# Performance work log

Hardware: AMD Instinct MI355X
Metric: run time of the kernel (lower is better)

Reference implementation:

```python
import jax, jax.numpy as jnp
import numpy as np

NUM_HEADS = 16
HEAD_DIM = 64  # hidden_dim 1024 / 16 heads
COH_DIM = 8
MOT_RANK = 4


def _linear(x, W, b):
    # torch nn.Linear: y = x @ W.T + b
    return jnp.einsum('...i,oi->...o', x, W) + b


def setup_inputs() -> dict:
    key = jax.random.key(0)
    ks = jax.random.split(key, 17)
    d, c, m = HEAD_DIM, COH_DIM, MOT_RANK
    s = 1.0 / np.sqrt(d)
    sc = 1.0 / np.sqrt(c)
    sm = 1.0 / np.sqrt(m)
    inp = {
        'x': jax.random.normal(ks[0], (4, 2048, 1024), dtype=jnp.float32),
        'Wi': jax.random.uniform(ks[1], (d, d), jnp.float32, -s, s),
        'bi': jax.random.uniform(ks[2], (d,), jnp.float32, -s, s),
        'Wq': jax.random.uniform(ks[3], (d, d), jnp.float32, -s, s),
        'bq': jax.random.uniform(ks[4], (d,), jnp.float32, -s, s),
        'Wk': jax.random.uniform(ks[5], (d, d), jnp.float32, -s, s),
        'bk': jax.random.uniform(ks[6], (d,), jnp.float32, -s, s),
        'Wv': jax.random.uniform(ks[7], (d, d), jnp.float32, -s, s),
        'bv': jax.random.uniform(ks[8], (d,), jnp.float32, -s, s),
        'Wc': jax.random.uniform(ks[9], (c, d), jnp.float32, -s, s),
        'bc': jax.random.uniform(ks[10], (c,), jnp.float32, -s, s),
        'Wci': jax.random.uniform(ks[11], (d, c), jnp.float32, -sc, sc),
        'bci': jax.random.uniform(ks[12], (d,), jnp.float32, -sc, sc),
        'Wm': jax.random.uniform(ks[13], (m, d), jnp.float32, -s, s),
        'bm': jax.random.uniform(ks[14], (m,), jnp.float32, -s, s),
        'Wmi': jax.random.uniform(ks[15], (d, m), jnp.float32, -sm, sm),
        'bmi': jax.random.uniform(ks[16], (d,), jnp.float32, -sm, sm),
    }
    return inp


def reference(x, Wi, bi, Wq, bq, Wk, bk, Wv, bv, Wc, bc, Wci, bci, Wm, bm, Wmi, bmi):
    B, S, D = x.shape
    H, hd = NUM_HEADS, HEAD_DIM
    # split heads: [B, H, S, hd]
    xh = x.reshape(B, S, H, hd).transpose(0, 2, 1, 3)
    # resolution * load_factor = 1.0 scaling (identity here), then input projection
    h = _linear(xh, Wi, bi)
    q = _linear(h, Wq, bq)
    k = _linear(h, Wk, bk)
    v = _linear(h, Wv, bv)
    # scaled dot-product attention per head
    scores = jnp.einsum('bhqd,bhkd->bhqk', q, k) / jnp.sqrt(jnp.float32(hd))
    attn = jax.nn.softmax(scores, axis=-1)
    out = jnp.einsum('bhqk,bhkd->bhqd', attn, v)
    # cohomology round-trip projection
    out = _linear(_linear(out, Wc, bc), Wci, bci)
    # motive round-trip projection
    out = _linear(_linear(out, Wm, bm), Wmi, bmi)
    # merge heads back to [B, S, D]
    return out.transpose(0, 2, 1, 3).reshape(B, S, D)
```

## Files before the change

### kernel.cpp

```cpp
#include <hip/hip_runtime.h>


#define SEQ 2048
#define DM  1024
#define HD  64
#define QS  0.180336880111120429f

typedef short bf16x8 __attribute__((ext_vector_type(8)));
typedef unsigned short u16x8 __attribute__((ext_vector_type(8)));
typedef float f32x16 __attribute__((ext_vector_type(16)));

#define MFMA32 __builtin_amdgcn_mfma_f32_32x32x16_bf16

#if defined(__has_builtin)
#if __has_builtin(__builtin_amdgcn_exp2f)
#define EXP2(x) __builtin_amdgcn_exp2f(x)
#endif
#endif
#ifndef EXP2
#define EXP2(x) exp2f(x)
#endif

#define KG_OFF  12288
#define VG_OFF  (12288 + 8388608)
#define WS_NEED ((size_t)512 + 2ull * (12288 + 2ull * 8388608))

__device__ __forceinline__ unsigned short f2bf(float f) {
    unsigned int v = __float_as_uint(f);
    unsigned int r = v + 0x7FFFu + ((v >> 16) & 1u);
    return (unsigned short)(r >> 16);
}
__device__ __forceinline__ unsigned int pk2r(float a, float b) {
    return __builtin_amdgcn_perm(__float_as_uint(b) + 0x8000u,
                                 __float_as_uint(a) + 0x8000u, 0x07060302u);
}
__device__ __forceinline__ unsigned int pk2t(float a, float b) {
    return __builtin_amdgcn_perm(__float_as_uint(b), __float_as_uint(a), 0x07060302u);
}
__device__ __forceinline__ f32x16 z16() {
    f32x16 v;
    #pragma unroll
    for (int i = 0; i < 16; i++) v[i] = 0.f;
    return v;
}

__device__ __forceinline__ void mm16L(const float* __restrict__ wrow,
                                      const float* __restrict__ L, int i0,
                                      float* __restrict__ acc) {
    #pragma unroll
    for (int ii = 0; ii < 16; ii++) acc[ii] = 0.f;
    for (int t = 0; t < 64; t += 4) {
        float4 w4 = *(const float4*)(wrow + t);
        #pragma unroll
        for (int d = 0; d < 4; d++) {
            float wv = (d == 0) ? w4.x : (d == 1) ? w4.y : (d == 2) ? w4.z : w4.w;
            const float* lr = L + (t + d) * 68 + i0;
            float4 a = *(const float4*)lr;
            float4 b = *(const float4*)(lr + 4);
            float4 c = *(const float4*)(lr + 8);
            float4 e = *(const float4*)(lr + 12);
            acc[0] += wv * a.x;  acc[1] += wv * a.y;  acc[2]  += wv * a.z;  acc[3]  += wv * a.w;
            acc[4] += wv * b.x;  acc[5] += wv * b.y;  acc[6]  += wv * b.z;  acc[7]  += wv * b.w;
            acc[8] += wv * c.x;  acc[9] += wv * c.y;  acc[10] += wv * c.z;  acc[11] += wv * c.w;
            acc[12] += wv * e.x; acc[13] += wv * e.y; acc[14] += wv * e.z;  acc[15] += wv * e.w;
        }
    }
}

__global__ __launch_bounds__(256)
void qmt_combine(const float* __restrict__ Wi,  const float* __restrict__ bi,
                 const float* __restrict__ Wq,  const float* __restrict__ bq,
                 const float* __restrict__ Wk,  const float* __restrict__ bk,
                 const float* __restrict__ Wv,  const float* __restrict__ bv,
                 const float* __restrict__ Wc,  const float* __restrict__ bc,
                 const float* __restrict__ Wci, const float* __restrict__ bci,
                 const float* __restrict__ Wm,  const float* __restrict__ bm,
                 const float* __restrict__ Wmi, const float* __restrict__ bmi,
                 float* __restrict__ ws) {
    const int tid = threadIdx.x;
    const int o = tid & 63;
    const int i0 = (tid >> 6) * 16;
    const bool lead = (tid < 64);

    __shared__ float Wi_s[64 * 68];
    __shared__ float Wq_s[64 * 68];
    __shared__ float Wk_s[64 * 68];
    __shared__ float Wv_s[64 * 68];
    __shared__ float Wvi_s[64 * 68];
    __shared__ float M_s[64 * 68];
    __shared__ float Wc_s[512];
    __shared__ float Wci_s[512];
    __shared__ float Wm_s[256];
    __shared__ float Wmi_s[256];
    __shared__ float bi_s[64], bvi_s[64], c1[64], c2[4];
    __shared__ float U1[32], U2[256];

    unsigned short* wsu = (unsigned short*)(ws + 128);

    for (int i4 = tid; i4 < 1024; i4 += 256) {
        int r = i4 >> 4, c = (i4 & 15) * 4;
        *(float4*)&Wi_s[r * 68 + c] = *(const float4*)(Wi + i4 * 4);
        *(float4*)&Wq_s[r * 68 + c] = *(const float4*)(Wq + i4 * 4);
        *(float4*)&Wk_s[r * 68 + c] = *(const float4*)(Wk + i4 * 4);
        *(float4*)&Wv_s[r * 68 + c] = *(const float4*)(Wv + i4 * 4);
    }
    if (tid < 128) {
        *(float4*)&Wc_s[tid * 4]  = *(const float4*)(Wc + tid * 4);
        *(float4*)&Wci_s[tid * 4] = *(const float4*)(Wci + tid * 4);
    } else if (tid < 192) {
        int t = tid - 128;
        *(float4*)&Wm_s[t * 4]  = *(const float4*)(Wm + t * 4);
        *(float4*)&Wmi_s[t * 4] = *(const float4*)(Wmi + t * 4);
    }
    if (lead) bi_s[o] = bi[o];
    __syncthreads();

    float acc[16];
    mm16L(Wq_s + o * 68, Wi_s, i0, acc);
    #pragma unroll
    for (int ii = 0; ii < 16; ii++) wsu[o * 64 + i0 + ii] = f2bf(acc[ii] * QS);
    if (lead) {
        float s = bq[o];
        for (int t = 0; t < 64; t++) s += Wq_s[o * 68 + t] * bi_s[t];
        ws[o] = s * QS;
    }
    mm16L(Wk_s + o * 68, Wi_s, i0, acc);
    #pragma unroll
    for (int ii = 0; ii < 16; ii++) wsu[4096 + o * 64 + i0 + ii] = f2bf(acc[ii]);
    mm16L(Wv_s + o * 68, Wi_s, i0, acc);
    #pragma unroll
    for (int ii = 0; ii < 16; ii++) Wvi_s[o * 68 + i0 + ii] = acc[ii];
    if (lead) {
        float s = bv[o];
        for (int t = 0; t < 64; t++) s += Wv_s[o * 68 + t] * bi_s[t];
        bvi_s[o] = s;
    }
    if (tid < 32) {
        int a = tid >> 3, c = tid & 7;
        float s = 0.f;
        for (int t = 0; t < 64; t++) s += Wm_s[a * 64 + t] * Wci_s[t * 8 + c];
        U1[a * 8 + c] = s;
    }
    __syncthreads();
    if (lead) {
        for (int a = 0; a < 4; a++) {
            float s = 0.f;
            for (int cc = 0; cc < 8; cc++) s += U1[a * 8 + cc] * Wc_s[cc * 64 + o];
            U2[a * 64 + o] = s;
        }
        float s = bci[o];
        for (int j = 0; j < 8; j++) s += Wci_s[o * 8 + j] * bc[j];
        c1[o] = s;
    }
    __syncthreads();
    #pragma unroll
    for (int ii = 0; ii < 16; ii++) {
        float s = 0.f;
        for (int a = 0; a < 4; a++) s += Wmi_s[o * 4 + a] * U2[a * 64 + i0 + ii];
        M_s[o * 68 + i0 + ii] = s;
    }
    if (tid < 4) {
        float s = bm[tid];
        for (int i = 0; i < 64; i++) s += Wm_s[tid * 64 + i] * c1[i];
        c2[tid] = s;
    }
    __syncthreads();
    mm16L(M_s + o * 68, Wvi_s, i0, acc);
    #pragma unroll
    for (int ii = 0; ii < 16; ii++) wsu[8192 + o * 64 + i0 + ii] = f2bf(acc[ii]);
    if (lead) {
        float bvv = 0.f;
        for (int t = 0; t < 64; t++) bvv += M_s[o * 68 + t] * bvi_s[t];
        float cvv = bmi[o];
        for (int a = 0; a < 4; a++) cvv += Wmi_s[o * 4 + a] * c2[a];
        ws[64 + o] = cvv + bvv;
    }
}

__global__ __launch_bounds__(256)
void qmt_kv(const float* __restrict__ x, float* __restrict__ ws) {
    const int tid = threadIdx.x;
    const int w = tid >> 6;
    const int lane = tid & 63;
    const int ln = lane & 31;
    const int h = lane >> 5;
    const int b = blockIdx.y >> 4;
    const int hh = blockIdx.y & 15;

    const unsigned short* wsu = (const unsigned short*)(ws + 128);
    unsigned short* Kg = (unsigned short*)(ws + 128) + KG_OFF + (size_t)blockIdx.y * (2048 * 64);
    unsigned short* Vg = (unsigned short*)(ws + 128) + VG_OFF + (size_t)blockIdx.y * (64 * 2048);

    const int krl = (w >> 1) * 32 + ln;
    const int dt32 = (w & 1) * 32;

    bf16x8 akf[4], avf[4];
    #pragma unroll
    for (int c = 0; c < 4; c++) {
        int row = dt32 + ln;
        int col = c * 16 + h * 8;
        akf[c] = *(const bf16x8*)(wsu + 4096 + row * 64 + col);
        avf[c] = *(const bf16x8*)(wsu + 8192 + row * 64 + col);
    }
    for (int t = 0; t < 4; t++) {
        const int kt = blockIdx.x * 4 + t;
        bf16x8 xf[4];
        const float* xr = x + ((size_t)(b * SEQ + kt * 64 + krl) * DM + hh * HD);
        #pragma unroll
        for (int c = 0; c < 4; c++) {
            const float* p = xr + c * 16 + h * 8;
            float4 f0 = *(const float4*)p;
            float4 f1 = *(const float4*)(p + 4);
            union { bf16x8 v; unsigned int u[4]; } tt;
            tt.u[0] = pk2t(f0.x, f0.y); tt.u[1] = pk2t(f0.z, f0.w);
            tt.u[2] = pk2t(f1.x, f1.y); tt.u[3] = pk2t(f1.z, f1.w);
            xf[c] = tt.v;
        }
        f32x16 kacc = z16(), vacc = z16();
        #pragma unroll
        for (int c = 0; c < 4; c++) kacc = MFMA32(akf[c], xf[c], kacc, 0, 0, 0);
        #pragma unroll
        for (int c = 0; c < 4; c++) vacc = MFMA32(xf[c], avf[c], vacc, 0, 0, 0);
        #pragma unroll
        for (int g = 0; g < 4; g++) {
            uint2 pk_, pv_;
            pk_.x = pk2r(kacc[4 * g + 0], kacc[4 * g + 1]);
            pk_.y = pk2r(kacc[4 * g + 2], kacc[4 * g + 3]);
            *(uint2*)&Kg[(size_t)(kt * 64 + krl) * 64 + dt32 + 8 * g + 4 * h] = pk_;
            pv_.x = pk2r(vacc[4 * g + 0], vacc[4 * g + 1]);
            pv_.y = pk2r(vacc[4 * g + 2], vacc[4 * g + 3]);
            *(uint2*)&Vg[(size_t)(dt32 + ln) * 2048 + kt * 64 + (w >> 1) * 32 + 8 * g + 4 * h] = pv_;
        }
    }
}

__global__ __launch_bounds__(256, 4)
void qmt_attn2(const float* __restrict__ x, const float* __restrict__ wsf,
               float* __restrict__ out) {
    __shared__ __align__(16) unsigned short ps_s[128 * 72];
    __shared__ __align__(16) unsigned short ks_s[64 * 72];
    __shared__ __align__(16) unsigned short vt_s[64 * 72];
    __shared__ float als_l[128];
    __shared__ float ls_l[128];

    const int tid = threadIdx.x;
    const int w = tid >> 6;
    const int lane = tid & 63;
    const int ln = lane & 31;
    const int h = lane >> 5;
    const int b = blockIdx.y >> 4;
    const int hh = blockIdx.y & 15;
    const int qbase = blockIdx.x * 128;

    const unsigned short* wsu = (const unsigned short*)(wsf + 128);
    const unsigned short* Kg = wsu + KG_OFF + (size_t)blockIdx.y * (2048 * 64);
    const unsigned short* Vg = wsu + VG_OFF + (size_t)blockIdx.y * (64 * 2048);

    const float ec0 = wsf[64 + ln];
    const float ec1 = wsf[96 + ln];

    bf16x8 qf[4];
    {
        bf16x8 xq[4];
        const float* xrow = x + ((size_t)(b * SEQ + qbase + w * 32 + ln) * DM + hh * HD);
        #pragma unroll
        for (int c = 0; c < 4; c++) {
            const float* p = xrow + c * 16 + h * 8;
            float4 f0 = *(const float4*)p;
            float4 f1 = *(const float4*)(p + 4);
            union { bf16x8 v; unsigned int u[4]; } t;
            t.u[0] = pk2t(f0.x, f0.y); t.u[1] = pk2t(f0.z, f0.w);
            t.u[2] = pk2t(f1.x, f1.y); t.u[3] = pk2t(f1.z, f1.w);
            xq[c] = t.v;
        }
        #pragma unroll
        for (int m = 0; m < 2; m++) {
            f32x16 acc;
            #pragma unroll
            for (int g = 0; g < 4; g++) {
                float4 b4 = *(const float4*)&wsf[m * 32 + 8 * g + 4 * h];
                acc[4 * g + 0] = b4.x; acc[4 * g + 1] = b4.y;
                acc[4 * g + 2] = b4.z; acc[4 * g + 3] = b4.w;
            }
            #pragma unroll
            for (int c = 0; c < 4; c++) {
                bf16x8 aq = *(const bf16x8*)(wsu + (m * 32 + ln) * 64 + c * 16 + h * 8);
                acc = MFMA32(aq, xq[c], acc, 0, 0, 0);
            }
            #pragma unroll
            for (int g = 0; g < 4; g++) {
                uint2 pw;
                pw.x = pk2r(acc[4 * g + 0], acc[4 * g + 1]);
                pw.y = pk2r(acc[4 * g + 2], acc[4 * g + 3]);
                *(uint2*)&ps_s[(w * 32 + ln) * 72 + m * 32 + 8 * g + 4 * h] = pw;
            }
        }
        #pragma unroll
        for (int c = 0; c < 4; c++)
            qf[c] = *(const bf16x8*)&ps_s[(w * 32 + ln) * 72 + c * 16 + h * 8];
    }

    f32x16 o0 = z16(), o1 = z16();
    float m_i = -1e30f, l_i = 0.f;

    const int srow = tid >> 3;
    const int scol = (tid & 7) * 8;

    u16x8 ka, kb, va, vb;
    ka = *(const u16x8*)(Kg + (size_t)srow * 64 + scol);
    kb = *(const u16x8*)(Kg + (size_t)(srow + 32) * 64 + scol);
    va = *(const u16x8*)(Vg + (size_t)srow * 2048 + scol);
    vb = *(const u16x8*)(Vg + (size_t)(srow + 32) * 2048 + scol);
    *(u16x8*)&ks_s[srow * 72 + scol] = ka;
    *(u16x8*)&ks_s[(srow + 32) * 72 + scol] = kb;
    *(u16x8*)&vt_s[srow * 72 + scol] = va;
    *(u16x8*)&vt_s[(srow + 32) * 72 + scol] = vb;
    __syncthreads();

    for (int kt = 0; kt < SEQ / 64; kt++) {
        const bool more = (kt < SEQ / 64 - 1);
        if (more) {
            const int kn = (kt + 1) * 64;
            ka = *(const u16x8*)(Kg + (size_t)(kn + srow) * 64 + scol);
            kb = *(const u16x8*)(Kg + (size_t)(kn + srow + 32) * 64 + scol);
            va = *(const u16x8*)(Vg + (size_t)srow * 2048 + kn + scol);
            vb = *(const u16x8*)(Vg + (size_t)(srow + 32) * 2048 + kn + scol);
        }

        f32x16 st0 = z16(), st1 = z16();
        #pragma unroll
        for (int c = 0; c < 4; c++) {
            bf16x8 k0 = *(const bf16x8*)&ks_s[ln * 72 + c * 16 + h * 8];
            bf16x8 k1 = *(const bf16x8*)&ks_s[(32 + ln) * 72 + c * 16 + h * 8];
            st0 = MFMA32(k0, qf[c], st0, 0, 0, 0);
            st1 = MFMA32(k1, qf[c], st1, 0, 0, 0);
        }
        float mx = st0[0];
        #pragma unroll
        for (int i = 1; i < 16; i++) mx = fmaxf(mx, st0[i]);
        #pragma unroll
        for (int i = 0; i < 16; i++) mx = fmaxf(mx, st1[i]);
        mx = fmaxf(mx, __shfl_xor(mx, 32));
        const float mn = fmaxf(m_i, mx);
        const float al = EXP2(m_i - mn);
        float ss = 0.f;
        #pragma unroll
        for (int i = 0; i < 16; i++) { st0[i] = EXP2(st0[i] - mn); ss += st0[i]; }
        #pragma unroll
        for (int i = 0; i < 16; i++) { st1[i] = EXP2(st1[i] - mn); ss += st1[i]; }
        ss += __shfl_xor(ss, 32);
        l_i = l_i * al + ss;
        m_i = mn;
        if (lane < 32) als_l[w * 32 + lane] = al;
        #pragma unroll
        for (int g = 0; g < 4; g++) {
            uint2 p0, p1;
            p0.x = pk2r(st0[4 * g + 0], st0[4 * g + 1]);
            p0.y = pk2r(st0[4 * g + 2], st0[4 * g + 3]);
            *(uint2*)&ps_s[(w * 32 + ln) * 72 + 8 * g + 4 * h] = p0;
            p1.x = pk2r(st1[4 * g + 0], st1[4 * g + 1]);
            p1.y = pk2r(st1[4 * g + 2], st1[4 * g + 3]);
            *(uint2*)&ps_s[(w * 32 + ln) * 72 + 32 + 8 * g + 4 * h] = p1;
        }
        #pragma unroll
        for (int g = 0; g < 4; g++) {
            float4 a4 = *(const float4*)&als_l[w * 32 + 8 * g + 4 * h];
            o0[4 * g + 0] *= a4.x; o0[4 * g + 1] *= a4.y;
            o0[4 * g + 2] *= a4.z; o0[4 * g + 3] *= a4.w;
            o1[4 * g + 0] *= a4.x; o1[4 * g + 1] *= a4.y;
            o1[4 * g + 2] *= a4.z; o1[4 * g + 3] *= a4.w;
        }
        #pragma unroll
        for (int c = 0; c < 4; c++) {
            bf16x8 pf = *(const bf16x8*)&ps_s[(w * 32 + ln) * 72 + c * 16 + h * 8];
            bf16x8 v0 = *(const bf16x8*)&vt_s[ln * 72 + c * 16 + h * 8];
            bf16x8 v1 = *(const bf16x8*)&vt_s[(32 + ln) * 72 + c * 16 + h * 8];
            o0 = MFMA32(pf, v0, o0, 0, 0, 0);
            o1 = MFMA32(pf, v1, o1, 0, 0, 0);
        }
        __syncthreads();
        if (more) {
            *(u16x8*)&ks_s[srow * 72 + scol] = ka;
            *(u16x8*)&ks_s[(srow + 32) * 72 + scol] = kb;
            *(u16x8*)&vt_s[srow * 72 + scol] = va;
            *(u16x8*)&vt_s[(srow + 32) * 72 + scol] = vb;
        }
        __syncthreads();
    }

    if (lane < 32) ls_l[w * 32 + lane] = l_i;
    #pragma unroll
    for (int g = 0; g < 4; g++) {
        float4 l4 = *(const float4*)&ls_l[w * 32 + 8 * g + 4 * h];
        float4 iv = make_float4(1.f / l4.x, 1.f / l4.y, 1.f / l4.z, 1.f / l4.w);
        #pragma unroll
        for (int i = 0; i < 4; i++) {
            float ivv = (i == 0) ? iv.x : (i == 1) ? iv.y : (i == 2) ? iv.z : iv.w;
            int q = qbase + w * 32 + 8 * g + 4 * h + i;
            float* orow = out + ((size_t)(b * SEQ + q) * DM + hh * HD);
            orow[ln] = o0[4 * g + i] * ivv + ec0;
            orow[32 + ln] = o1[4 * g + i] * ivv + ec1;
        }
    }
}

__global__ __launch_bounds__(256, 3)
void qmt_attn_fb(const float* __restrict__ x, const float* __restrict__ wsf,
                 float* __restrict__ out) {
    __shared__ __align__(16) unsigned short ps_s[128 * 72];
    __shared__ __align__(16) unsigned short ks_s[64 * 72];
    __shared__ __align__(16) unsigned short vt_s[64 * 72];
    __shared__ float als_l[128];
    __shared__ float ls_l[128];

    const int tid = threadIdx.x;
    const int w = tid >> 6;
    const int lane = tid & 63;
    const int ln = lane & 31;
    const int h = lane >> 5;
    const int b = blockIdx.y >> 4;
    const int hh = blockIdx.y & 15;
    const int qbase = blockIdx.x * 128;

    const unsigned short* wsu = (const unsigned short*)(wsf + 128);

    bf16x8 akf[4], avf[4];
    #pragma unroll
    for (int c = 0; c < 4; c++) {
        int row = (w & 1) * 32 + ln;
        int col = c * 16 + h * 8;
        akf[c] = *(const bf16x8*)(wsu + 4096 + row * 64 + col);
        avf[c] = *(const bf16x8*)(wsu + 8192 + row * 64 + col);
    }
    const float ec0 = wsf[64 + ln];
    const float ec1 = wsf[96 + ln];

    bf16x8 qf[4];
    {
        bf16x8 xq[4];
        const float* xrow = x + ((size_t)(b * SEQ + qbase + w * 32 + ln) * DM + hh * HD);
        #pragma unroll
        for (int c = 0; c < 4; c++) {
            const float* p = xrow + c * 16 + h * 8;
            float4 f0 = *(const float4*)p;
            float4 f1 = *(const float4*)(p + 4);
            union { bf16x8 v; unsigned int u[4]; } t;
            t.u[0] = pk2t(f0.x, f0.y); t.u[1] = pk2t(f0.z, f0.w);
            t.u[2] = pk2t(f1.x, f1.y); t.u[3] = pk2t(f1.z, f1.w);
            xq[c] = t.v;
        }
        #pragma unroll
        for (int m = 0; m < 2; m++) {
            f32x16 acc;
            #pragma unroll
            for (int g = 0; g < 4; g++) {
                float4 b4 = *(const float4*)&wsf[m * 32 + 8 * g + 4 * h];
                acc[4 * g + 0] = b4.x; acc[4 * g + 1] = b4.y;
                acc[4 * g + 2] = b4.z; acc[4 * g + 3] = b4.w;
            }
            #pragma unroll
            for (int c = 0; c < 4; c++) {
                bf16x8 aq = *(const bf16x8*)(wsu + (m * 32 + ln) * 64 + c * 16 + h * 8);
                acc = MFMA32(aq, xq[c], acc, 0, 0, 0);
            }
            #pragma unroll
            for (int g = 0; g < 4; g++) {
                uint2 pw;
                pw.x = pk2r(acc[4 * g + 0], acc[4 * g + 1]);
                pw.y = pk2r(acc[4 * g + 2], acc[4 * g + 3]);
                *(uint2*)&ps_s[(w * 32 + ln) * 72 + m * 32 + 8 * g + 4 * h] = pw;
            }
        }
        #pragma unroll
        for (int c = 0; c < 4; c++)
            qf[c] = *(const bf16x8*)&ps_s[(w * 32 + ln) * 72 + c * 16 + h * 8];
    }

    f32x16 o0 = z16(), o1 = z16();
    float m_i = -1e30f, l_i = 0.f;

    const int krl = (w >> 1) * 32 + ln;
    const int dt32 = (w & 1) * 32;

    for (int kt = 0; kt < SEQ / 64; kt++) {
        bf16x8 xf[4];
        const float* xr = x + ((size_t)(b * SEQ + kt * 64 + krl) * DM + hh * HD);
        #pragma unroll
        for (int c = 0; c < 4; c++) {
            const float* p = xr + c * 16 + h * 8;
            float4 f0 = *(const float4*)p;
            float4 f1 = *(const float4*)(p + 4);
            union { bf16x8 v; unsigned int u[4]; } t;
            t.u[0] = pk2t(f0.x, f0.y); t.u[1] = pk2t(f0.z, f0.w);
            t.u[2] = pk2t(f1.x, f1.y); t.u[3] = pk2t(f1.z, f1.w);
            xf[c] = t.v;
        }
        f32x16 kacc = z16(), vacc = z16();
        #pragma unroll
        for (int c = 0; c < 4; c++) kacc = MFMA32(akf[c], xf[c], kacc, 0, 0, 0);
        #pragma unroll
        for (int c = 0; c < 4; c++) vacc = MFMA32(xf[c], avf[c], vacc, 0, 0, 0);
        #pragma unroll
        for (int g = 0; g < 4; g++) {
            uint2 pk_, pv_;
            pk_.x = pk2r(kacc[4 * g + 0], kacc[4 * g + 1]);
            pk_.y = pk2r(kacc[4 * g + 2], kacc[4 * g + 3]);
            *(uint2*)&ks_s[krl * 72 + dt32 + 8 * g + 4 * h] = pk_;
            pv_.x = pk2r(vacc[4 * g + 0], vacc[4 * g + 1]);
            pv_.y = pk2r(vacc[4 * g + 2], vacc[4 * g + 3]);
            *(uint2*)&vt_s[(dt32 + ln) * 72 + (w >> 1) * 32 + 8 * g + 4 * h] = pv_;
        }
        __syncthreads();

        f32x16 st0 = z16(), st1 = z16();
        #pragma unroll
        for (int c = 0; c < 4; c++) {
            bf16x8 k0 = *(const bf16x8*)&ks_s[ln * 72 + c * 16 + h * 8];
            bf16x8 k1 = *(const bf16x8*)&ks_s[(32 + ln) * 72 + c * 16 + h * 8];
            st0 = MFMA32(k0, qf[c], st0, 0, 0, 0);
            st1 = MFMA32(k1, qf[c], st1, 0, 0, 0);
        }
        float mx = st0[0];
        #pragma unroll
        for (int i = 1; i < 16; i++) mx = fmaxf(mx, st0[i]);
        #pragma unroll
        for (int i = 0; i < 16; i++) mx = fmaxf(mx, st1[i]);
        mx = fmaxf(mx, __shfl_xor(mx, 32));
        const float mn = fmaxf(m_i, mx);
        const float al = EXP2(m_i - mn);
        float ss = 0.f;
        #pragma unroll
        for (int i = 0; i < 16; i++) { st0[i] = EXP2(st0[i] - mn); ss += st0[i]; }
        #pragma unroll
        for (int i = 0; i < 16; i++) { st1[i] = EXP2(st1[i] - mn); ss += st1[i]; }
        ss += __shfl_xor(ss, 32);
        l_i = l_i * al + ss;
        m_i = mn;
        if (lane < 32) als_l[w * 32 + lane] = al;
        #pragma unroll
        for (int g = 0; g < 4; g++) {
            uint2 p0, p1;
            p0.x = pk2r(st0[4 * g + 0], st0[4 * g + 1]);
            p0.y = pk2r(st0[4 * g + 2], st0[4 * g + 3]);
            *(uint2*)&ps_s[(w * 32 + ln) * 72 + 8 * g + 4 * h] = p0;
            p1.x = pk2r(st1[4 * g + 0], st1[4 * g + 1]);
            p1.y = pk2r(st1[4 * g + 2], st1[4 * g + 3]);
            *(uint2*)&ps_s[(w * 32 + ln) * 72 + 32 + 8 * g + 4 * h] = p1;
        }
        #pragma unroll
        for (int g = 0; g < 4; g++) {
            float4 a4 = *(const float4*)&als_l[w * 32 + 8 * g + 4 * h];
            o0[4 * g + 0] *= a4.x; o0[4 * g + 1] *= a4.y;
            o0[4 * g + 2] *= a4.z; o0[4 * g + 3] *= a4.w;
            o1[4 * g + 0] *= a4.x; o1[4 * g + 1] *= a4.y;
            o1[4 * g + 2] *= a4.z; o1[4 * g + 3] *= a4.w;
        }
        #pragma unroll
        for (int c = 0; c < 4; c++) {
            bf16x8 pf = *(const bf16x8*)&ps_s[(w * 32 + ln) * 72 + c * 16 + h * 8];
            bf16x8 v0 = *(const bf16x8*)&vt_s[ln * 72 + c * 16 + h * 8];
            bf16x8 v1 = *(const bf16x8*)&vt_s[(32 + ln) * 72 + c * 16 + h * 8];
            o0 = MFMA32(pf, v0, o0, 0, 0, 0);
            o1 = MFMA32(pf, v1, o1, 0, 0, 0);
        }
        __syncthreads();
    }

    if (lane < 32) ls_l[w * 32 + lane] = l_i;
    #pragma unroll
    for (int g = 0; g < 4; g++) {
        float4 l4 = *(const float4*)&ls_l[w * 32 + 8 * g + 4 * h];
        float4 iv = make_float4(1.f / l4.x, 1.f / l4.y, 1.f / l4.z, 1.f / l4.w);
        #pragma unroll
        for (int i = 0; i < 4; i++) {
            float ivv = (i == 0) ? iv.x : (i == 1) ? iv.y : (i == 2) ? iv.z : iv.w;
            int q = qbase + w * 32 + 8 * g + 4 * h + i;
            float* orow = out + ((size_t)(b * SEQ + q) * DM + hh * HD);
            orow[ln] = o0[4 * g + i] * ivv + ec0;
            orow[32 + ln] = o1[4 * g + i] * ivv + ec1;
        }
    }
}

extern "C" void kernel_launch(void* const* d_in, const int* in_sizes, int n_in,
                              void* d_out, int out_size, void* d_ws, size_t ws_size,
                              hipStream_t stream) {
    const float* x = (const float*)d_in[0];
    float* wsf = (float*)d_ws;

    qmt_combine<<<1, 256, 0, stream>>>(
        (const float*)d_in[1],  (const float*)d_in[2],
        (const float*)d_in[3],  (const float*)d_in[4],
        (const float*)d_in[5],  (const float*)d_in[6],
        (const float*)d_in[7],  (const float*)d_in[8],
        (const float*)d_in[9],  (const float*)d_in[10],
        (const float*)d_in[11], (const float*)d_in[12],
        (const float*)d_in[13], (const float*)d_in[14],
        (const float*)d_in[15], (const float*)d_in[16],
        wsf);

    if (ws_size >= WS_NEED) {
        dim3 gkv(SEQ / 256, 64);
        qmt_kv<<<gkv, 256, 0, stream>>>(x, wsf);
        dim3 grid(SEQ / 128, 64);
        qmt_attn2<<<grid, 256, 0, stream>>>(x, wsf, (float*)d_out);
    } else {
        dim3 grid(SEQ / 128, 64);
        qmt_attn_fb<<<grid, 256, 0, stream>>>(x, wsf, (float*)d_out);
    }
}
```

Before: 247.2 us.

## Rework attention kernel: register P/Q fragments, lazy rescale, swizzled LDS, split combine

The main attention kernel now keeps Q and P fragments in registers, using hardware bf16 pack plus permlane32 swaps, instead of round-tripping them through shared memory. It skips the output rescale unless the running max grows past a threshold, and swaps padded K/V tiles for XOR-swizzled ones. It also splits the weight-combine kernel across three blocks and launches the K/V projection with one tile per block. These changes target LDS traffic, per-tile exp/rescale work and serial prologue latency, at the cost of inline asm that depends on the gfx950 instruction set and a thresholded softmax max that changes rounding behaviour.

After: 243.1 us. About the same (-1.7%).

```diff
diff --git a/kernel.cpp b/kernel.cpp
--- a/kernel.cpp
+++ b/kernel.cpp
@@ -5,6 +5,7 @@
 #define DM  1024
 #define HD  64
 #define QS  0.180336880111120429f
+#define THR 8.0f
 
 typedef short bf16x8 __attribute__((ext_vector_type(8)));
 typedef unsigned short u16x8 __attribute__((ext_vector_type(8)));
@@ -37,11 +38,30 @@
 __device__ __forceinline__ unsigned int pk2t(float a, float b) {
     return __builtin_amdgcn_perm(__float_as_uint(b), __float_as_uint(a), 0x07060302u);
 }
+__device__ __forceinline__ unsigned int cvtpk(float a, float b) {
+    unsigned int r;
+    asm("v_cvt_pk_bf16_f32 %0, %1, %2" : "=v"(r) : "v"(a), "v"(b));
+    return r;
+}
+__device__ __forceinline__ void swap32(unsigned int& a, unsigned int& b) {
+    asm("v_permlane32_swap_b32 %0, %1" : "+v"(a), "+v"(b));
+}
 __device__ __forceinline__ f32x16 z16() {
     f32x16 v;
     #pragma unroll
     for (int i = 0; i < 16; i++) v[i] = 0.f;
     return v;
+}
+
+__device__ __forceinline__ void pack2(const f32x16 s, bf16x8& fA, bf16x8& fB) {
+    union { bf16x8 v; unsigned int u[4]; } a, b;
+    a.u[0] = cvtpk(s[0], s[1]);   a.u[1] = cvtpk(s[2], s[3]);
+    a.u[2] = cvtpk(s[4], s[5]);   a.u[3] = cvtpk(s[6], s[7]);
+    b.u[0] = cvtpk(s[8], s[9]);   b.u[1] = cvtpk(s[10], s[11]);
+    b.u[2] = cvtpk(s[12], s[13]); b.u[3] = cvtpk(s[14], s[15]);
+    swap32(a.u[0], a.u[2]); swap32(a.u[1], a.u[3]);
+    swap32(b.u[0], b.u[2]); swap32(b.u[1], b.u[3]);
+    fA = a.v; fB = b.v;
 }
 
 __device__ __forceinline__ void mm16L(const float* __restrict__ wrow,
@@ -81,11 +101,10 @@
     const int o = tid & 63;
     const int i0 = (tid >> 6) * 16;
     const bool lead = (tid < 64);
-
+    const int role = blockIdx.x;
+
+    __shared__ float Wa_s[64 * 68];
     __shared__ float Wi_s[64 * 68];
-    __shared__ float Wq_s[64 * 68];
-    __shared__ float Wk_s[64 * 68];
-    __shared__ float Wv_s[64 * 68];
     __shared__ float Wvi_s[64 * 68];
     __shared__ float M_s[64 * 68];
     __shared__ float Wc_s[512];
@@ -96,43 +115,50 @@
     __shared__ float U1[32], U2[256];
 
     unsigned short* wsu = (unsigned short*)(ws + 128);
+    const float* Wa = (role == 0) ? Wq : (role == 1) ? Wk : Wv;
 
     for (int i4 = tid; i4 < 1024; i4 += 256) {
         int r = i4 >> 4, c = (i4 & 15) * 4;
         *(float4*)&Wi_s[r * 68 + c] = *(const float4*)(Wi + i4 * 4);
-        *(float4*)&Wq_s[r * 68 + c] = *(const float4*)(Wq + i4 * 4);
-        *(float4*)&Wk_s[r * 68 + c] = *(const float4*)(Wk + i4 * 4);
-        *(float4*)&Wv_s[r * 68 + c] = *(const float4*)(Wv + i4 * 4);
-    }
-    if (tid < 128) {
-        *(float4*)&Wc_s[tid * 4]  = *(const float4*)(Wc + tid * 4);
-        *(float4*)&Wci_s[tid * 4] = *(const float4*)(Wci + tid * 4);
-    } else if (tid < 192) {
-        int t = tid - 128;
-        *(float4*)&Wm_s[t * 4]  = *(const float4*)(Wm + t * 4);
-        *(float4*)&Wmi_s[t * 4] = *(const float4*)(Wmi + t * 4);
+        *(float4*)&Wa_s[r * 68 + c] = *(const float4*)(Wa + i4 * 4);
+    }
+    if (role == 2) {
+        if (tid < 128) {
+            *(float4*)&Wc_s[tid * 4]  = *(const float4*)(Wc + tid * 4);
+            *(float4*)&Wci_s[tid * 4] = *(const float4*)(Wci + tid * 4);
+        } else if (tid < 192) {
+            int t = tid - 128;
+            *(float4*)&Wm_s[t * 4]  = *(const float4*)(Wm + t * 4);
+            *(float4*)&Wmi_s[t * 4] = *(const float4*)(Wmi + t * 4);
+        }
     }
     if (lead) bi_s[o] = bi[o];
     __syncthreads();
 
     float acc[16];
-    mm16L(Wq_s + o * 68, Wi_s, i0, acc);
-    #pragma unroll
-    for (int ii = 0; ii < 16; ii++) wsu[o * 64 + i0 + ii] = f2bf(acc[ii] * QS);
-    if (lead) {
-        float s = bq[o];
-        for (int t = 0; t < 64; t++) s += Wq_s[o * 68 + t] * bi_s[t];
-        ws[o] = s * QS;
-    }
-    mm16L(Wk_s + o * 68, Wi_s, i0, acc);
-    #pragma unroll
-    for (int ii = 0; ii < 16; ii++) wsu[4096 + o * 64 + i0 + ii] = f2bf(acc[ii]);
-    mm16L(Wv_s + o * 68, Wi_s, i0, acc);
+    if (role == 0) {
+        mm16L(Wa_s + o * 68, Wi_s, i0, acc);
+        #pragma unroll
+        for (int ii = 0; ii < 16; ii++) wsu[o * 64 + i0 + ii] = f2bf(acc[ii] * QS);
+        if (lead) {
+            float s = bq[o];
+            for (int t = 0; t < 64; t++) s += Wa_s[o * 68 + t] * bi_s[t];
+            ws[o] = s * QS;
+        }
+        return;
+    }
+    if (role == 1) {
+        mm16L(Wa_s + o * 68, Wi_s, i0, acc);
+        #pragma unroll
+        for (int ii = 0; ii < 16; ii++) wsu[4096 + o * 64 + i0 + ii] = f2bf(acc[ii]);
+        return;
+    }
+    mm16L(Wa_s + o * 68, Wi_s, i0, acc);
     #pragma unroll
     for (int ii = 0; ii < 16; ii++) Wvi_s[o * 68 + i0 + ii] = acc[ii];
     if (lead) {
         float s = bv[o];
-        for (int t = 0; t < 64; t++) s += Wv_s[o * 68 + t] * bi_s[t];
+        for (int t = 0; t < 64; t++) s += Wa_s[o * 68 + t] * bi_s[t];
         bvi_s[o] = s;
     }
     if (tid < 32) {
@@ -186,6 +212,7 @@
     const int h = lane >> 5;
     const int b = blockIdx.y >> 4;
     const int hh = blockIdx.y & 15;
+    const int kt = blockIdx.x;
 
     const unsigned short* wsu = (const unsigned short*)(ws + 128);
     unsigned short* Kg = (unsigned short*)(ws + 128) + KG_OFF + (size_t)blockIdx.y * (2048 * 64);
@@ -202,44 +229,40 @@
         akf[c] = *(const bf16x8*)(wsu + 4096 + row * 64 + col);
         avf[c] = *(const bf16x8*)(wsu + 8192 + row * 64 + col);
     }
-    for (int t = 0; t < 4; t++) {
-        const int kt = blockIdx.x * 4 + t;
-        bf16x8 xf[4];
-        const float* xr = x + ((size_t)(b * SEQ + kt * 64 + krl) * DM + hh * HD);
-        #pragma unroll
-        for (int c = 0; c < 4; c++) {
-            const float* p = xr + c * 16 + h * 8;
-            float4 f0 = *(const float4*)p;
-            float4 f1 = *(const float4*)(p + 4);
-            union { bf16x8 v; unsigned int u[4]; } tt;
-            tt.u[0] = pk2t(f0.x, f0.y); tt.u[1] = pk2t(f0.z, f0.w);
-            tt.u[2] = pk2t(f1.x, f1.y); tt.u[3] = pk2t(f1.z, f1.w);
-            xf[c] = tt.v;
-        }
-        f32x16 kacc = z16(), vacc = z16();
-        #pragma unroll
-        for (int c = 0; c < 4; c++) kacc = MFMA32(akf[c], xf[c], kacc, 0, 0, 0);
-        #pragma unroll
-        for (int c = 0; c < 4; c++) vacc = MFMA32(xf[c], avf[c], vacc, 0, 0, 0);
-        #pragma unroll
-        for (int g = 0; g < 4; g++) {
-            uint2 pk_, pv_;
-            pk_.x = pk2r(kacc[4 * g + 0], kacc[4 * g + 1]);
-            pk_.y = pk2r(kacc[4 * g + 2], kacc[4 * g + 3]);
-            *(uint2*)&Kg[(size_t)(kt * 64 + krl) * 64 + dt32 + 8 * g + 4 * h] = pk_;
-            pv_.x = pk2r(vacc[4 * g + 0], vacc[4 * g + 1]);
-            pv_.y = pk2r(vacc[4 * g + 2], vacc[4 * g + 3]);
-            *(uint2*)&Vg[(size_t)(dt32 + ln) * 2048 + kt * 64 + (w >> 1) * 32 + 8 * g + 4 * h] = pv_;
-        }
+    bf16x8 xf[4];
+    const float* xr = x + ((size_t)(b * SEQ + kt * 64 + krl) * DM + hh * HD);
+    #pragma unroll
+    for (int c = 0; c < 4; c++) {
+        const float* p = xr + c * 16 + h * 8;
+        float4 f0 = *(const float4*)p;
+        float4 f1 = *(const float4*)(p + 4);
+        union { bf16x8 v; unsigned int u[4]; } tt;
+        tt.u[0] = pk2t(f0.x, f0.y); tt.u[1] = pk2t(f0.z, f0.w);
+        tt.u[2] = pk2t(f1.x, f1.y); tt.u[3] = pk2t(f1.z, f1.w);
+        xf[c] = tt.v;
+    }
+    f32x16 kacc = z16(), vacc = z16();
+    #pragma unroll
+    for (int c = 0; c < 4; c++) kacc = MFMA32(akf[c], xf[c], kacc, 0, 0, 0);
+    #pragma unroll
+    for (int c = 0; c < 4; c++) vacc = MFMA32(xf[c], avf[c], vacc, 0, 0, 0);
+    #pragma unroll
+    for (int g = 0; g < 4; g++) {
+        uint2 pk_, pv_;
+        pk_.x = cvtpk(kacc[4 * g + 0], kacc[4 * g + 1]);
+        pk_.y = cvtpk(kacc[4 * g + 2], kacc[4 * g + 3]);
+        *(uint2*)&Kg[(size_t)(kt * 64 + krl) * 64 + dt32 + 8 * g + 4 * h] = pk_;
+        pv_.x = cvtpk(vacc[4 * g + 0], vacc[4 * g + 1]);
+        pv_.y = cvtpk(vacc[4 * g + 2], vacc[4 * g + 3]);
+        *(uint2*)&Vg[(size_t)(dt32 + ln) * 2048 + kt * 64 + (w >> 1) * 32 + 8 * g + 4 * h] = pv_;
     }
 }
 
 __global__ __launch_bounds__(256, 4)
 void qmt_attn2(const float* __restrict__ x, const float* __restrict__ wsf,
                float* __restrict__ out) {
-    __shared__ __align__(16) unsigned short ps_s[128 * 72];
-    __shared__ __align__(16) unsigned short ks_s[64 * 72];
-    __shared__ __align__(16) unsigned short vt_s[64 * 72];
+    __shared__ __align__(16) unsigned short ks_s[64 * 64];
+    __shared__ __align__(16) unsigned short vt_s[64 * 64];
     __shared__ float als_l[128];
     __shared__ float ls_l[128];
 
@@ -256,6 +279,189 @@
     const unsigned short* Kg = wsu + KG_OFF + (size_t)blockIdx.y * (2048 * 64);
     const unsigned short* Vg = wsu + VG_OFF + (size_t)blockIdx.y * (64 * 2048);
 
+    const float ec0 = wsf[64 + ln];
+    const float ec1 = wsf[96 + ln];
+
+    const int srow = tid >> 3;
+    const int scol = (tid & 7) * 8;
+    const int sch = (((tid & 7) ^ (srow & 7)) * 8);
+    const int swm = ln & 7;
+
+    u16x8 ka = *(const u16x8*)(Kg + (size_t)srow * 64 + scol);
+    u16x8 kb = *(const u16x8*)(Kg + (size_t)(srow + 32) * 64 + scol);
+    u16x8 va = *(const u16x8*)(Vg + (size_t)srow * 2048 + scol);
+    u16x8 vb = *(const u16x8*)(Vg + (size_t)(srow + 32) * 2048 + scol);
+
+    bf16x8 qf[4];
+    {
+        bf16x8 xq[4];
+        const float* xrow = x + ((size_t)(b * SEQ + qbase + w * 32 + ln) * DM + hh * HD);
+        #pragma unroll
+        for (int c = 0; c < 4; c++) {
+            const float* p = xrow + c * 16 + h * 8;
+            float4 f0 = *(const float4*)p;
+            float4 f1 = *(const float4*)(p + 4);
+            union { bf16x8 v; unsigned int u[4]; } t;
+            t.u[0] = pk2t(f0.x, f0.y); t.u[1] = pk2t(f0.z, f0.w);
+            t.u[2] = pk2t(f1.x, f1.y); t.u[3] = pk2t(f1.z, f1.w);
+            xq[c] = t.v;
+        }
+        #pragma unroll
+        for (int m = 0; m < 2; m++) {
+            f32x16 acc;
+            #pragma unroll
+            for (int g = 0; g < 4; g++) {
+                float4 b4 = *(const float4*)&wsf[m * 32 + 8 * g + 4 * h];
+                acc[4 * g + 0] = b4.x; acc[4 * g + 1] = b4.y;
+                acc[4 * g + 2] = b4.z; acc[4 * g + 3] = b4.w;
+            }
+            #pragma unroll
+            for (int c = 0; c < 4; c++) {
+                bf16x8 aq = *(const bf16x8*)(wsu + (m * 32 + ln) * 64 + c * 16 + h * 8);
+                acc = MFMA32(aq, xq[c], acc, 0, 0, 0);
+            }
+            pack2(acc, qf[2 * m], qf[2 * m + 1]);
+        }
+    }
+
+    f32x16 o0 = z16(), o1 = z16();
+    float m_i = -1e30f, l_i = 0.f;
+
+    *(u16x8*)&ks_s[srow * 64 + sch] = ka;
+    *(u16x8*)&ks_s[(srow + 32) * 64 + sch] = kb;
+    *(u16x8*)&vt_s[srow * 64 + sch] = va;
+    *(u16x8*)&vt_s[(srow + 32) * 64 + sch] = vb;
+    __syncthreads();
+
+    for (int kt = 0; kt < SEQ / 64; kt++) {
+        const bool more = (kt < SEQ / 64 - 1);
+        if (more) {
+            const int kn = (kt + 1) * 64;
+            ka = *(const u16x8*)(Kg + (size_t)(kn + srow) * 64 + scol);
+            kb = *(const u16x8*)(Kg + (size_t)(kn + srow + 32) * 64 + scol);
+            va = *(const u16x8*)(Vg + (size_t)srow * 2048 + kn + scol);
+            vb = *(const u16x8*)(Vg + (size_t)(srow + 32) * 2048 + kn + scol);
+        }
+
+        f32x16 st0 = z16(), st1 = z16();
+        #pragma unroll
+        for (int c = 0; c < 4; c++) {
+            const int ci = ((c * 2 + h) ^ swm) * 8;
+            bf16x8 k0 = *(const bf16x8*)&ks_s[ln * 64 + ci];
+            bf16x8 k1 = *(const bf16x8*)&ks_s[(32 + ln) * 64 + ci];
+            st0 = MFMA32(k0, qf[c], st0, 0, 0, 0);
+            st1 = MFMA32(k1, qf[c], st1, 0, 0, 0);
+        }
+
+        float tm[8];
+        #pragma unroll
+        for (int i = 0; i < 8; i++)
+            tm[i] = fmaxf(fmaxf(st0[i], st0[i + 8]), fmaxf(st1[i], st1[i + 8]));
+        #pragma unroll
+        for (int i = 0; i < 4; i++) tm[i] = fmaxf(tm[i], tm[i + 4]);
+        float mx = fmaxf(fmaxf(tm[0], tm[1]), fmaxf(tm[2], tm[3]));
+        mx = fmaxf(mx, __shfl_xor(mx, 32));
+
+        const bool need = __any(mx > m_i + THR) != 0;
+        float mn = m_i, al = 1.0f;
+        if (need) {
+            mn = fmaxf(m_i, mx);
+            al = EXP2(m_i - mn);
+            if (lane < 32) als_l[w * 32 + lane] = al;
+        }
+
+        #pragma unroll
+        for (int i = 0; i < 16; i++) st0[i] = EXP2(st0[i] - mn);
+        #pragma unroll
+        for (int i = 0; i < 16; i++) st1[i] = EXP2(st1[i] - mn);
+        float sm[8];
+        #pragma unroll
+        for (int i = 0; i < 8; i++)
+            sm[i] = (st0[i] + st0[i + 8]) + (st1[i] + st1[i + 8]);
+        #pragma unroll
+        for (int i = 0; i < 4; i++) sm[i] += sm[i + 4];
+        float ss = (sm[0] + sm[1]) + (sm[2] + sm[3]);
+        ss += __shfl_xor(ss, 32);
+        l_i = l_i * al + ss;
+        m_i = mn;
+
+        bf16x8 pf[4];
+        pack2(st0, pf[0], pf[1]);
+        pack2(st1, pf[2], pf[3]);
+
+        if (need) {
+            #pragma unroll
+            for (int g = 0; g < 4; g++) {
+                float4 a4 = *(const float4*)&als_l[w * 32 + 8 * g + 4 * h];
+                o0[4 * g + 0] *= a4.x; o0[4 * g + 1] *= a4.y;
+                o0[4 * g + 2] *= a4.z; o0[4 * g + 3] *= a4.w;
+                o1[4 * g + 0] *= a4.x; o1[4 * g + 1] *= a4.y;
+                o1[4 * g + 2] *= a4.z; o1[4 * g + 3] *= a4.w;
+            }
+        }
+
+        #pragma unroll
+        for (int c = 0; c < 4; c++) {
+            const int ci = ((c * 2 + h) ^ swm) * 8;
+            bf16x8 v0 = *(const bf16x8*)&vt_s[ln * 64 + ci];
+            bf16x8 v1 = *(const bf16x8*)&vt_s[(32 + ln) * 64 + ci];
+            o0 = MFMA32(pf[c], v0, o0, 0, 0, 0);
+            o1 = MFMA32(pf[c], v1, o1, 0, 0, 0);
+        }
+        __syncthreads();
+        if (more) {
+            *(u16x8*)&ks_s[srow * 64 + sch] = ka;
+            *(u16x8*)&ks_s[(srow + 32) * 64 + sch] = kb;
+            *(u16x8*)&vt_s[srow * 64 + sch] = va;
+            *(u16x8*)&vt_s[(srow + 32) * 64 + sch] = vb;
+        }
+        __syncthreads();
+    }
+
+    if (lane < 32) ls_l[w * 32 + lane] = l_i;
+    #pragma unroll
+    for (int g = 0; g < 4; g++) {
+        float4 l4 = *(const float4*)&ls_l[w * 32 + 8 * g + 4 * h];
+        float4 iv = make_float4(1.f / l4.x, 1.f / l4.y, 1.f / l4.z, 1.f / l4.w);
+        #pragma unroll
+        for (int i = 0; i < 4; i++) {
+            float ivv = (i == 0) ? iv.x : (i == 1) ? iv.y : (i == 2) ? iv.z : iv.w;
+            int q = qbase + w * 32 + 8 * g + 4 * h + i;
+            float* orow = out + ((size_t)(b * SEQ + q) * DM + hh * HD);
+            orow[ln] = o0[4 * g + i] * ivv + ec0;
+            orow[32 + ln] = o1[4 * g + i] * ivv + ec1;
+        }
+    }
+}
+
+__global__ __launch_bounds__(256, 3)
+void qmt_attn_fb(const float* __restrict__ x, const float* __restrict__ wsf,
+                 float* __restrict__ out) {
+    __shared__ __align__(16) unsigned short ps_s[128 * 72];
+    __shared__ __align__(16) unsigned short ks_s[64 * 72];
+    __shared__ __align__(16) unsigned short vt_s[64 * 72];
+    __shared__ float als_l[128];
+    __shared__ float ls_l[128];
+
+    const int tid = threadIdx.x;
+    const int w = tid >> 6;
+    const int lane = tid & 63;
+    const int ln = lane & 31;
+    const int h = lane >> 5;
+    const int b = blockIdx.y >> 4;
+    const int hh = blockIdx.y & 15;
+    const int qbase = blockIdx.x * 128;
+
+    const unsigned short* wsu = (const unsigned short*)(wsf + 128);
+
+    bf16x8 akf[4], avf[4];
+    #pragma unroll
+    for (int c = 0; c < 4; c++) {
+        int row = (w & 1) * 32 + ln;
+        int col = c * 16 + h * 8;
+        akf[c] = *(const bf16x8*)(wsu + 4096 + row * 64 + col);
+        avf[c] = *(const bf16x8*)(wsu + 8192 + row * 64 + col);
+    }
     const float ec0 = wsf[64 + ln];
     const float ec1 = wsf[96 + ln];
 
@@ -303,29 +509,38 @@
     f32x16 o0 = z16(), o1 = z16();
     float m_i = -1e30f, l_i = 0.f;
 
-    const int srow = tid >> 3;
-    const int scol = (tid & 7) * 8;
-
-    u16x8 ka, kb, va, vb;
-    ka = *(const u16x8*)(Kg + (size_t)srow * 64 + scol);
-    kb = *(const u16x8*)(Kg + (size_t)(srow + 32) * 64 + scol);
-    va = *(const u16x8*)(Vg + (size_t)srow * 2048 + scol);
-    vb = *(const u16x8*)(Vg + (size_t)(srow + 32) * 2048 + scol);
-    *(u16x8*)&ks_s[srow * 72 + scol] = ka;
-    *(u16x8*)&ks_s[(srow + 32) * 72 + scol] = kb;
-    *(u16x8*)&vt_s[srow * 72 + scol] = va;
-    *(u16x8*)&vt_s[(srow + 32) * 72 + scol] = vb;
-    __syncthreads();
+    const int krl = (w >> 1) * 32 + ln;
+    const int dt32 = (w & 1) * 32;
 
     for (int kt = 0; kt < SEQ / 64; kt++) {
-        const bool more = (kt < SEQ / 64 - 1);
-        if (more) {
-            const int kn = (kt + 1) * 64;
-            ka = *(const u16x8*)(Kg + (size_t)(kn + srow) * 64 + scol);
-            kb = *(const u16x8*)(Kg + (size_t)(kn + srow + 32) * 64 + scol);
-            va = *(const u16x8*)(Vg + (size_t)srow * 2048 + kn + scol);
-            vb = *(const u16x8*)(Vg + (size_t)(srow + 32) * 2048 + kn + scol);
-        }
+        bf16x8 xf[4];
+        const float* xr = x + ((size_t)(b * SEQ + kt * 64 + krl) * DM + hh * HD);
+        #pragma unroll
+        for (int c = 0; c < 4; c++) {
+            const float* p = xr + c * 16 + h * 8;
+            float4 f0 = *(const float4*)p;
+            float4 f1 = *(const float4*)(p + 4);
+            union { bf16x8 v; unsigned int u[4]; } t;
+            t.u[0] = pk2t(f0.x, f0.y); t.u[1] = pk2t(f0.z, f0.w);
+            t.u[2] = pk2t(f1.x, f1.y); t.u[3] = pk2t(f1.z, f1.w);
+            xf[c] = t.v;
+        }
+        f32x16 kacc = z16(), vacc = z16();
+        #pragma unroll
+        for (int c = 0; c < 4; c++) kacc = MFMA32(akf[c], xf[c], kacc, 0, 0, 0);
+        #pragma unroll
+        for (int c = 0; c < 4; c++) vacc = MFMA32(xf[c], avf[c], vacc, 0, 0, 0);
+        #pragma unroll
+        for (int g = 0; g < 4; g++) {
+            uint2 pk_, pv_;
+            pk_.x = pk2r(kacc[4 * g + 0], kacc[4 * g + 1]);
+            pk_.y = pk2r(kacc[4 * g + 2], kacc[4 * g + 3]);
+            *(uint2*)&ks_s[krl * 72 + dt32 + 8 * g + 4 * h] = pk_;
+            pv_.x = pk2r(vacc[4 * g + 0], vacc[4 * g + 1]);
+            pv_.y = pk2r(vacc[4 * g + 2], vacc[4 * g + 3]);
+            *(uint2*)&vt_s[(dt32 + ln) * 72 + (w >> 1) * 32 + 8 * g + 4 * h] = pv_;
+        }
+        __syncthreads();
 
         f32x16 st0 = z16(), st1 = z16();
         #pragma unroll
@@ -379,13 +594,6 @@
             o1 = MFMA32(pf, v1, o1, 0, 0, 0);
         }
         __syncthreads();
-        if (more) {
-            *(u16x8*)&ks_s[srow * 72 + scol] = ka;
-            *(u16x8*)&ks_s[(srow + 32) * 72 + scol] = kb;
-            *(u16x8*)&vt_s[srow * 72 + scol] = va;
-            *(u16x8*)&vt_s[(srow + 32) * 72 + scol] = vb;
-        }
-        __syncthreads();
     }
 
     if (lane < 32) ls_l[w * 32 + lane] = l_i;
@@ -404,191 +612,13 @@
     }
 }
 
-__global__ __launch_bounds__(256, 3)
-void qmt_attn_fb(const float* __restrict__ x, const float* __restrict__ wsf,
-                 float* __restrict__ out) {
-    __shared__ __align__(16) unsigned short ps_s[128 * 72];
-    __shared__ __align__(16) unsigned short ks_s[64 * 72];
-    __shared__ __align__(16) unsigned short vt_s[64 * 72];
-    __shared__ float als_l[128];
-    __shared__ float ls_l[128];
-
-    const int tid = threadIdx.x;
-    const int w = tid >> 6;
-    const int lane = tid & 63;
-    const int ln = lane & 31;
-    const int h = lane >> 5;
-    const int b = blockIdx.y >> 4;
-    const int hh = blockIdx.y & 15;
-    const int qbase = blockIdx.x * 128;
-
-    const unsigned short* wsu = (const unsigned short*)(wsf + 128);
-
-    bf16x8 akf[4], avf[4];
-    #pragma unroll
-    for (int c = 0; c < 4; c++) {
-        int row = (w & 1) * 32 + ln;
-        int col = c * 16 + h * 8;
-        akf[c] = *(const bf16x8*)(wsu + 4096 + row * 64 + col);
-        avf[c] = *(const bf16x8*)(wsu + 8192 + row * 64 + col);
-    }
-    const float ec0 = wsf[64 + ln];
-    const float ec1 = wsf[96 + ln];
-
-    bf16x8 qf[4];
-    {
-        bf16x8 xq[4];
-        const float* xrow = x + ((size_t)(b * SEQ + qbase + w * 32 + ln) * DM + hh * HD);
-        #pragma unroll
-        for (int c = 0; c < 4; c++) {
-            const float* p = xrow + c * 16 + h * 8;
-            float4 f0 = *(const float4*)p;
-            float4 f1 = *(const float4*)(p + 4);
-            union { bf16x8 v; unsigned int u[4]; } t;
-            t.u[0] = pk2t(f0.x, f0.y); t.u[1] = pk2t(f0.z, f0.w);
-            t.u[2] = pk2t(f1.x, f1.y); t.u[3] = pk2t(f1.z, f1.w);
-            xq[c] = t.v;
-        }
-        #pragma unroll
-        for (int m = 0; m < 2; m++) {
-            f32x16 acc;
-            #pragma unroll
-            for (int g = 0; g < 4; g++) {
-                float4 b4 = *(const float4*)&wsf[m * 32 + 8 * g + 4 * h];
-                acc[4 * g + 0] = b4.x; acc[4 * g + 1] = b4.y;
-                acc[4 * g + 2] = b4.z; acc[4 * g + 3] = b4.w;
-            }
-            #pragma unroll
-            for (int c = 0; c < 4; c++) {
-                bf16x8 aq = *(const bf16x8*)(wsu + (m * 32 + ln) * 64 + c * 16 + h * 8);
-                acc = MFMA32(aq, xq[c], acc, 0, 0, 0);
-            }
-            #pragma unroll
-            for (int g = 0; g < 4; g++) {
-                uint2 pw;
-                pw.x = pk2r(acc[4 * g + 0], acc[4 * g + 1]);
-                pw.y = pk2r(acc[4 * g + 2], acc[4 * g + 3]);
-                *(uint2*)&ps_s[(w * 32 + ln) * 72 + m * 32 + 8 * g + 4 * h] = pw;
-            }
-        }
-        #pragma unroll
-        for (int c = 0; c < 4; c++)
-            qf[c] = *(const bf16x8*)&ps_s[(w * 32 + ln) * 72 + c * 16 + h * 8];
-    }
-
-    f32x16 o0 = z16(), o1 = z16();
-    float m_i = -1e30f, l_i = 0.f;
-
-    const int krl = (w >> 1) * 32 + ln;
-    const int dt32 = (w & 1) * 32;
-
-    for (int kt = 0; kt < SEQ / 64; kt++) {
-        bf16x8 xf[4];
-        const float* xr = x + ((size_t)(b * SEQ + kt * 64 + krl) * DM + hh * HD);
-        #pragma unroll
-        for (int c = 0; c < 4; c++) {
-            const float* p = xr + c * 16 + h * 8;
-            float4 f0 = *(const float4*)p;
-            float4 f1 = *(const float4*)(p + 4);
-            union { bf16x8 v; unsigned int u[4]; } t;
-            t.u[0] = pk2t(f0.x, f0.y); t.u[1] = pk2t(f0.z, f0.w);
-            t.u[2] = pk2t(f1.x, f1.y); t.u[3] = pk2t(f1.z, f1.w);
-            xf[c] = t.v;
-        }
-        f32x16 kacc = z16(), vacc = z16();
-        #pragma unroll
-        for (int c = 0; c < 4; c++) kacc = MFMA32(akf[c], xf[c], kacc, 0, 0, 0);
-        #pragma unroll
-        for (int c = 0; c < 4; c++) vacc = MFMA32(xf[c], avf[c], vacc, 0, 0, 0);
-        #pragma unroll
-        for (int g = 0; g < 4; g++) {
-            uint2 pk_, pv_;
-            pk_.x = pk2r(kacc[4 * g + 0], kacc[4 * g + 1]);
-            pk_.y = pk2r(kacc[4 * g + 2], kacc[4 * g + 3]);
-            *(uint2*)&ks_s[krl * 72 + dt32 + 8 * g + 4 * h] = pk_;
-            pv_.x = pk2r(vacc[4 * g + 0], vacc[4 * g + 1]);
-            pv_.y = pk2r(vacc[4 * g + 2], vacc[4 * g + 3]);
-            *(uint2*)&vt_s[(dt32 + ln) * 72 + (w >> 1) * 32 + 8 * g + 4 * h] = pv_;
-        }
-        __syncthreads();
-
-        f32x16 st0 = z16(), st1 = z16();
-        #pragma unroll
-        for (int c = 0; c < 4; c++) {
-            bf16x8 k0 = *(const bf16x8*)&ks_s[ln * 72 + c * 16 + h * 8];
-            bf16x8 k1 = *(const bf16x8*)&ks_s[(32 + ln) * 72 + c * 16 + h * 8];
-            st0 = MFMA32(k0, qf[c], st0, 0, 0, 0);
-            st1 = MFMA32(k1, qf[c], st1, 0, 0, 0);
-        }
-        float mx = st0[0];
-        #pragma unroll
-        for (int i = 1; i < 16; i++) mx = fmaxf(mx, st0[i]);
-        #pragma unroll
-        for (int i = 0; i < 16; i++) mx = fmaxf(mx, st1[i]);
-        mx = fmaxf(mx, __shfl_xor(mx, 32));
-        const float mn = fmaxf(m_i, mx);
-        const float al = EXP2(m_i - mn);
-        float ss = 0.f;
-        #pragma unroll
-        for (int i = 0; i < 16; i++) { st0[i] = EXP2(st0[i] - mn); ss += st0[i]; }
-        #pragma unroll
-        for (int i = 0; i < 16; i++) { st1[i] = EXP2(st1[i] - mn); ss += st1[i]; }
-        ss += __shfl_xor(ss, 32);
-        l_i = l_i * al + ss;
-        m_i = mn;
-        if (lane < 32) als_l[w * 32 + lane] = al;
-        #pragma unroll
-        for (int g = 0; g < 4; g++) {
-            uint2 p0, p1;
-            p0.x = pk2r(st0[4 * g + 0], st0[4 * g + 1]);
-            p0.y = pk2r(st0[4 * g + 2], st0[4 * g + 3]);
-            *(uint2*)&ps_s[(w * 32 + ln) * 72 + 8 * g + 4 * h] = p0;
-            p1.x = pk2r(st1[4 * g + 0], st1[4 * g + 1]);
-            p1.y = pk2r(st1[4 * g + 2], st1[4 * g + 3]);
-            *(uint2*)&ps_s[(w * 32 + ln) * 72 + 32 + 8 * g + 4 * h] = p1;
-        }
-        #pragma unroll
-        for (int g = 0; g < 4; g++) {
-            float4 a4 = *(const float4*)&als_l[w * 32 + 8 * g + 4 * h];
-            o0[4 * g + 0] *= a4.x; o0[4 * g + 1] *= a4.y;
-            o0[4 * g + 2] *= a4.z; o0[4 * g + 3] *= a4.w;
-            o1[4 * g + 0] *= a4.x; o1[4 * g + 1] *= a4.y;
-            o1[4 * g + 2] *= a4.z; o1[4 * g + 3] *= a4.w;
-        }
-        #pragma unroll
-        for (int c = 0; c < 4; c++) {
-            bf16x8 pf = *(const bf16x8*)&ps_s[(w * 32 + ln) * 72 + c * 16 + h * 8];
-            bf16x8 v0 = *(const bf16x8*)&vt_s[ln * 72 + c * 16 + h * 8];
-            bf16x8 v1 = *(const bf16x8*)&vt_s[(32 + ln) * 72 + c * 16 + h * 8];
-            o0 = MFMA32(pf, v0, o0, 0, 0, 0);
-            o1 = MFMA32(pf, v1, o1, 0, 0, 0);
-        }
-        __syncthreads();
-    }
-
-    if (lane < 32) ls_l[w * 32 + lane] = l_i;
-    #pragma unroll
-    for (int g = 0; g < 4; g++) {
-        float4 l4 = *(const float4*)&ls_l[w * 32 + 8 * g + 4 * h];
-        float4 iv = make_float4(1.f / l4.x, 1.f / l4.y, 1.f / l4.z, 1.f / l4.w);
-        #pragma unroll
-        for (int i = 0; i < 4; i++) {
-            float ivv = (i == 0) ? iv.x : (i == 1) ? iv.y : (i == 2) ? iv.z : iv.w;
-            int q = qbase + w * 32 + 8 * g + 4 * h + i;
-            float* orow = out + ((size_t)(b * SEQ + q) * DM + hh * HD);
-            orow[ln] = o0[4 * g + i] * ivv + ec0;
-            orow[32 + ln] = o1[4 * g + i] * ivv + ec1;
-        }
-    }
-}
-
 extern "C" void kernel_launch(void* const* d_in, const int* in_sizes, int n_in,
                               void* d_out, int out_size, void* d_ws, size_t ws_size,
                               hipStream_t stream) {
     const float* x = (const float*)d_in[0];
     float* wsf = (float*)d_ws;
 
-    qmt_combine<<<1, 256, 0, stream>>>(
+    qmt_combine<<<3, 256, 0, stream>>>(
         (const float*)d_in[1],  (const float*)d_in[2],
         (const float*)d_in[3],  (const float*)d_in[4],
         (const float*)d_in[5],  (const float*)d_in[6],
@@ -600,7 +630,7 @@
         wsf);
 
     if (ws_size >= WS_NEED) {
-        dim3 gkv(SEQ / 256, 64);
+        dim3 gkv(SEQ / 64, 64);
         qmt_kv<<<gkv, 256, 0, stream>>>(x, wsf);
         dim3 grid(SEQ / 128, 64);
         qmt_attn2<<<grid, 256, 0, stream>>>(x, wsf, (float*)d_out);
```
